# Kernel optimization log

Measured on AMD Instinct MI355X. Metric: run time of the kernel, lower is better.

Reference implementation:

```python
import jax, jax.numpy as jnp
import numpy as np

B, NI, NA, D = 16, 2048, 2048, 256

def setup_inputs() -> dict:
    key = jax.random.key(0)
    k1, k2, k3 = jax.random.split(key, 3)
    input_seq = jax.random.normal(k1, (B, NI, D), dtype=jnp.float32)
    attendee_seq = jax.random.normal(k2, (B, NA, D), dtype=jnp.float32)
    # glorot-ish scale for bilinear weight
    W = jax.random.normal(k3, (D, D), dtype=jnp.float32) * (1.0 / np.sqrt(D))
    return {"input_seq": input_seq, "attendee_seq": attendee_seq, "W": W}

def reference(input_seq, attendee_seq, W):
    # bilinear scores: (x_i W) . a_j   -> [B, NI, NA]
    xW = jnp.einsum('bid,de->bie', input_seq, W)
    scores = jnp.einsum('bie,bje->bij', xW, attendee_seq)
    A = jax.nn.softmax(scores, axis=2)                 # softmax over attendee axis
    # weighted context: sum_j A[b,i,j] * v[b,j,:] -> [B, NI, D]
    attended = jnp.einsum('bij,bjd->bid', A, attendee_seq)
    return attended
```

## Files before the change

kernel.cpp:

```cpp
#include <hip/hip_runtime.h>
#include <hip/hip_bf16.h>

#define BB 16
#define NI 2048
#define NA 2048
#define DD 256
#define KVB 32
#define NT (NA / KVB)

typedef _Float16 half8 __attribute__((ext_vector_type(8)));
typedef __attribute__((ext_vector_type(4))) float f32x4;
typedef __attribute__((ext_vector_type(4))) unsigned int uint4v;

typedef const unsigned int CGU __attribute__((address_space(1)));
typedef unsigned int LU __attribute__((address_space(3)));

static __device__ __forceinline__ unsigned short f2h(float f) {
  union { _Float16 h; unsigned short u; } x; x.h = (_Float16)f; return x.u;
}
static __device__ __forceinline__ float h2f(unsigned short u) {
  union { _Float16 h; unsigned short u; } x; x.u = u; return (float)x.h;
}
static __device__ __forceinline__ unsigned int pk2(float a, float b) {
  return __builtin_bit_cast(unsigned int, __builtin_amdgcn_cvt_pkrtz(a, b));
}
static __device__ __forceinline__ float ex2(float x) {
  return __builtin_amdgcn_exp2f(x);
}
static __device__ __forceinline__ void gload16(const unsigned short* g, unsigned short* l) {
  __builtin_amdgcn_global_load_lds((CGU*)g, (LU*)l, 16, 0, 0);
}

__global__ void prep_kernel(const float* __restrict__ a,
                            unsigned short* __restrict__ kfrag,
                            unsigned short* __restrict__ vfrag,
                            const float* __restrict__ w,
                            unsigned short* __restrict__ wth,
                            unsigned short* __restrict__ wtl) {
  __shared__ float t[64][65];
  int bx = blockIdx.x;
  int tid = threadIdx.x;
  int rr = tid >> 4, c4 = tid & 15;

  if (bx >= 2048) {
    int r = bx - 2048;
    int dt = r >> 2, et = r & 3;
    int d0 = dt * 64, e0 = et * 64;
    int cc = c4 * 4;
#pragma unroll
    for (int k = 0; k < 4; ++k) {
      int row = rr + k * 16;
      float4 v = *(const float4*)(w + (size_t)(d0 + row) * DD + e0 + cc);
      t[row][cc + 0] = v.x; t[row][cc + 1] = v.y; t[row][cc + 2] = v.z; t[row][cc + 3] = v.w;
    }
    __syncthreads();
#pragma unroll
    for (int k = 0; k < 4; ++k) {
      int e = rr + k * 16;
      int eg = e0 + e;
      ushort4 h, l;
      float v0 = t[cc + 0][e]; h.x = f2h(v0); l.x = f2h(v0 - h2f(h.x));
      float v1 = t[cc + 1][e]; h.y = f2h(v1); l.y = f2h(v1 - h2f(h.y));
      float v2 = t[cc + 2][e]; h.z = f2h(v2); l.z = f2h(v2 - h2f(h.z));
      float v3 = t[cc + 3][e]; h.w = f2h(v3); l.w = f2h(v3 - h2f(h.w));
      int dd = d0 + cc;
      int u = dd >> 3, sub = dd & 7;
      size_t off = (size_t)eg * DD + ((u ^ (eg & 7)) * 8) + sub;
      *(ushort4*)(wth + off) = h;
      *(ushort4*)(wtl + off) = l;
    }
    return;
  }

  int b = bx >> 7;
  int r = bx & 127;
  int jt_t = r >> 2, dt_t = r & 3;
  int j0 = jt_t * 64, d0 = dt_t * 64;
#pragma unroll
  for (int k = 0; k < 4; ++k) {
    int row = rr + k * 16;
    int j = j0 + row;
    int d = d0 + c4 * 4;
    float4 v = *(const float4*)(a + ((size_t)b * NA + j) * DD + d);
    ushort4 hh;
    hh.x = f2h(v.x); hh.y = f2h(v.y); hh.z = f2h(v.z); hh.w = f2h(v.w);
    int kt = j >> 5, jtf = (j >> 4) & 1, l16k = j & 15;
    int c = d >> 5, quad = (d >> 3) & 3, e = d & 7;
    *(ushort4*)(kfrag + ((size_t)b * NT + kt) * 8192 + c * 1024 + jtf * 512 +
                (quad * 16 + l16k) * 8 + e) = hh;
    t[row][c4 * 4 + 0] = v.x; t[row][c4 * 4 + 1] = v.y;
    t[row][c4 * 4 + 2] = v.z; t[row][c4 * 4 + 3] = v.w;
  }
  __syncthreads();
#pragma unroll
  for (int k = 0; k < 4; ++k) {
    int dl = rr + k * 16;
    int d = d0 + dl;
    int j = j0 + c4 * 4;
    ushort4 o;
    o.x = f2h(t[c4 * 4 + 0][dl]); o.y = f2h(t[c4 * 4 + 1][dl]);
    o.z = f2h(t[c4 * 4 + 2][dl]); o.w = f2h(t[c4 * 4 + 3][dl]);
    int kt = j >> 5;
    int quad = c4 & 3;
    int jt = (c4 >> 2) & 1;
    int hh_ = (d >> 7) & 1, dtl = (d >> 4) & 7, l16v = d & 15;
    *(ushort4*)(vfrag + ((size_t)b * NT + kt) * 8192 + hh_ * 4096 + dtl * 512 +
                (quad * 16 + l16v) * 8 + jt * 4) = o;
  }
}

__global__ __launch_bounds__(256, 2) void qgemm_kernel(
    const float* __restrict__ x, const unsigned short* __restrict__ wth,
    const unsigned short* __restrict__ wtl, unsigned short* __restrict__ qf) {
  __shared__ unsigned short wb[2][64 * 256];
  const int tid = threadIdx.x;
  const int lane = tid & 63;
  const int wv = tid >> 6;
  const int quad = lane >> 4;
  const int l16 = lane & 15;
  const int m0 = blockIdx.x * 64;

  half8 xf[8];
  {
    const float* xr = x + (size_t)(m0 + wv * 16 + l16) * DD;
#pragma unroll
    for (int c = 0; c < 8; ++c) {
      float4 a = *(const float4*)(xr + c * 32 + quad * 8);
      float4 b = *(const float4*)(xr + c * 32 + quad * 8 + 4);
      half8 v;
      v[0] = (_Float16)a.x; v[1] = (_Float16)a.y; v[2] = (_Float16)a.z; v[3] = (_Float16)a.w;
      v[4] = (_Float16)b.x; v[5] = (_Float16)b.y; v[6] = (_Float16)b.z; v[7] = (_Float16)b.w;
      xf[c] = v;
    }
  }

#pragma unroll 1
  for (int eg = 0; eg < 4; ++eg) {
    uint4 t0[8], t1[8];
    {
      const unsigned short* sh = wth + (size_t)(eg * 64) * DD;
      const unsigned short* sl = wtl + (size_t)(eg * 64) * DD;
#pragma unroll
      for (int i = 0; i < 8; ++i) {
        t0[i] = *(const uint4*)(sh + (i * 256 + tid) * 8);
        t1[i] = *(const uint4*)(sl + (i * 256 + tid) * 8);
      }
    }
    __syncthreads();
#pragma unroll
    for (int i = 0; i < 8; ++i) {
      *(uint4*)(wb[0] + (i * 256 + tid) * 8) = t0[i];
      *(uint4*)(wb[1] + (i * 256 + tid) * 8) = t1[i];
    }
    __syncthreads();
#pragma unroll
    for (int etl = 0; etl < 4; ++etl) {
      int rloc = etl * 16 + l16;
      f32x4 acc; acc[0] = acc[1] = acc[2] = acc[3] = 0.f;
#pragma unroll
      for (int c = 0; c < 8; ++c) {
        int off = rloc * DD + (((4 * c + quad) ^ (rloc & 7)) * 8);
        half8 wh = *(const half8*)(wb[0] + off);
        half8 wl = *(const half8*)(wb[1] + off);
        acc = __builtin_amdgcn_mfma_f32_16x16x32_f16(xf[c], wh, acc, 0, 0, 0);
        acc = __builtin_amdgcn_mfma_f32_16x16x32_f16(xf[c], wl, acc, 0, 0, 0);
      }
      int e = eg * 64 + etl * 16 + l16;
#pragma unroll
      for (int rg = 0; rg < 4; ++rg) {
        qf[(size_t)(m0 + wv * 16 + 4 * quad + rg) * DD + e] = f2h(acc[rg] * 1.44269504f);
      }
    }
  }
}

__global__ __launch_bounds__(256, 4) void attn_kernel(
    const unsigned short* __restrict__ kfrag, const unsigned short* __restrict__ vfrag,
    const unsigned short* __restrict__ qf, float* __restrict__ out) {
  __shared__ unsigned short kls[2][KVB * DD];

  const int tid = threadIdx.x;
  const int lane = tid & 63;
  const int wv = tid >> 6;
  const int p = wv >> 1;
  const int h = wv & 1;
  const int quad = lane >> 4;
  const int l16 = lane & 15;

  int bx = blockIdx.x;
  int lbx = (bx & 7) * 128 + (bx >> 3);
  const int b = lbx >> 6;
  const int qbase = (lbx & 63) * 32 + p * 16;

  const unsigned short* kfb = kfrag + (size_t)b * NT * 8192;

  half8 qh[8];
  {
    const size_t qrow = ((size_t)b * NI + qbase + l16) * DD;
#pragma unroll
    for (int c = 0; c < 8; ++c)
      qh[c] = *(const half8*)(qf + qrow + c * 32 + quad * 8);
  }

  f32x4 acc[8];
#pragma unroll
  for (int dt = 0; dt < 8; ++dt) { acc[dt][0] = 0.f; acc[dt][1] = 0.f; acc[dt][2] = 0.f; acc[dt][3] = 0.f; }
  float m0r = -INFINITY;
  float l0 = 0.f;

  const unsigned short* vp = vfrag + (size_t)b * NT * 8192 + h * 4096 + lane * 8;
  const unsigned short* sp = kfb + 8192 + (wv * 512 + lane * 8);

#pragma unroll
  for (int i = 0; i < 4; ++i) {
    int off = (i * 4 + wv) * 512;
    gload16(kfb + off + lane * 8, &kls[0][off]);
  }
  __syncthreads();

#pragma unroll 1
  for (int kt = 0; kt < NT; ++kt) {
    half8 vb[8];
#pragma unroll
    for (int dt = 0; dt < 8; ++dt)
      vb[dt] = *(const half8*)(vp + dt * 512);

    if (kt + 1 < NT) {
      unsigned short* d = &kls[(kt + 1) & 1][wv * 512];
      gload16(sp + 0 * 2048, d + 0 * 2048);
      gload16(sp + 1 * 2048, d + 1 * 2048);
      gload16(sp + 2 * 2048, d + 2 * 2048);
      gload16(sp + 3 * 2048, d + 3 * 2048);
    }

    const unsigned short* kb = &kls[kt & 1][0];
    f32x4 st0, st1;
    st0[0] = st0[1] = st0[2] = st0[3] = 0.f;
    st1[0] = st1[1] = st1[2] = st1[3] = 0.f;
    __builtin_amdgcn_s_setprio(1);
#pragma unroll
    for (int c = 0; c < 8; ++c) {
      half8 k0 = *(const half8*)(kb + c * 1024 + lane * 8);
      half8 k1 = *(const half8*)(kb + c * 1024 + 512 + lane * 8);
      st0 = __builtin_amdgcn_mfma_f32_16x16x32_f16(k0, qh[c], st0, 0, 0, 0);
      st1 = __builtin_amdgcn_mfma_f32_16x16x32_f16(k1, qh[c], st1, 0, 0, 0);
    }
    __builtin_amdgcn_s_setprio(0);

    float mt = fmaxf(fmaxf(fmaxf(st0[0], st0[1]), fmaxf(st0[2], st0[3])),
                     fmaxf(fmaxf(st1[0], st1[1]), fmaxf(st1[2], st1[3])));
    if (__any(mt > m0r + 11.5416f)) {
      float mr = fmaxf(mt, __shfl_xor(mt, 16));
      mr = fmaxf(mr, __shfl_xor(mr, 32));
      float mn = fmaxf(m0r, mr);
      float sc = ex2(m0r - mn);
      l0 *= sc;
#pragma unroll
      for (int rg = 0; rg < 4; ++rg) {
        float a0 = __shfl(sc, 4 * quad + rg);
#pragma unroll
        for (int dt = 0; dt < 8; ++dt) acc[dt][rg] *= a0;
      }
      m0r = mn;
    }

    float e00 = ex2(st0[0] - m0r), e01 = ex2(st0[1] - m0r);
    float e02 = ex2(st0[2] - m0r), e03 = ex2(st0[3] - m0r);
    float e10 = ex2(st1[0] - m0r), e11 = ex2(st1[1] - m0r);
    float e12 = ex2(st1[2] - m0r), e13 = ex2(st1[3] - m0r);
    l0 += ((e00 + e01) + (e02 + e03)) + ((e10 + e11) + (e12 + e13));
    half8 pa;
    {
      uint4v pau = { pk2(e00, e01), pk2(e02, e03), pk2(e10, e11), pk2(e12, e13) };
      pa = __builtin_bit_cast(half8, pau);
    }

    __builtin_amdgcn_s_setprio(1);
#pragma unroll
    for (int dt = 0; dt < 8; ++dt)
      acc[dt] = __builtin_amdgcn_mfma_f32_16x16x32_f16(pa, vb[dt], acc[dt], 0, 0, 0);
    __builtin_amdgcn_s_setprio(0);

    vp += 8192;
    sp += 8192;
    __syncthreads();
  }

  l0 += __shfl_xor(l0, 16); l0 += __shfl_xor(l0, 32);
  float inv0 = 1.0f / l0;
  size_t ob = ((size_t)b * NI + qbase) * DD + h * 128;
#pragma unroll
  for (int rg = 0; rg < 4; ++rg) {
    float i0 = __shfl(inv0, 4 * quad + rg);
#pragma unroll
    for (int dt = 0; dt < 8; ++dt) {
      int d = dt * 16 + l16;
      out[ob + (size_t)(4 * quad + rg) * DD + d] = acc[dt][rg] * i0;
    }
  }
}

extern "C" void kernel_launch(void* const* d_in, const int* in_sizes, int n_in,
                              void* d_out, int out_size, void* d_ws, size_t ws_size,
                              hipStream_t stream) {
  const float* x = (const float*)d_in[0];
  const float* att = (const float*)d_in[1];
  const float* W = (const float*)d_in[2];
  float* out = (float*)d_out;

  const size_t NE = (size_t)BB * NA * DD;
  unsigned short* w0    = (unsigned short*)d_ws;
  unsigned short* kfrag = w0;
  unsigned short* vfrag = w0 + NE;
  unsigned short* qfp   = w0 + 2 * NE;
  unsigned short* wth   = w0 + 3 * NE;
  unsigned short* wtl   = w0 + 3 * NE + (size_t)DD * DD;

  prep_kernel<<<2064, 256, 0, stream>>>(att, kfrag, vfrag, W, wth, wtl);
  qgemm_kernel<<<512, 256, 0, stream>>>(x, wth, wtl, qfp);
  attn_kernel<<<1024, 256, 0, stream>>>(kfrag, vfrag, qfp, out);
}
```

Before: 197.6 us.

## Switch attention to 32x32x16 MFMA with 64-query blocks and new fragment layouts

Rewrites the attention inner loop to use 32x32x16 MFMA tiles instead of 16x16x32. Each wave now covers 32 query rows, so a block covers 64 queries and the grid halves to 512 blocks. The prep kernel writes K/V fragments in matching layouts, the softmax row-max needs fewer shuffles, and outputs are written as float4. Each K/V tile loaded into LDS now feeds twice as many queries, which cuts K/V traffic per query. In exchange, register pressure rises (16 Q fragments, 4x16 accumulators), occupancy drops to 2 blocks per CU, and the score reduction is split into two accumulators.

```diff
diff --git a/kernel.cpp b/kernel.cpp
--- a/kernel.cpp
+++ b/kernel.cpp
@@ -9,7 +9,7 @@
 #define NT (NA / KVB)
 
 typedef _Float16 half8 __attribute__((ext_vector_type(8)));
-typedef __attribute__((ext_vector_type(4))) float f32x4;
+typedef __attribute__((ext_vector_type(16))) float f32x16;
 typedef __attribute__((ext_vector_type(4))) unsigned int uint4v;
 
 typedef const unsigned int CGU __attribute__((address_space(1)));
@@ -84,10 +84,10 @@
     float4 v = *(const float4*)(a + ((size_t)b * NA + j) * DD + d);
     ushort4 hh;
     hh.x = f2h(v.x); hh.y = f2h(v.y); hh.z = f2h(v.z); hh.w = f2h(v.w);
-    int kt = j >> 5, jtf = (j >> 4) & 1, l16k = j & 15;
-    int c = d >> 5, quad = (d >> 3) & 3, e = d & 7;
-    *(ushort4*)(kfrag + ((size_t)b * NT + kt) * 8192 + c * 1024 + jtf * 512 +
-                (quad * 16 + l16k) * 8 + e) = hh;
+    int kt = j >> 5;
+    int ks = d >> 4;
+    int lk = (j & 31) + 32 * ((d >> 3) & 1);
+    *(ushort4*)(kfrag + (((size_t)b * NT + kt) * 16 + ks) * 512 + lk * 8 + (c4 & 1) * 4) = hh;
     t[row][c4 * 4 + 0] = v.x; t[row][c4 * 4 + 1] = v.y;
     t[row][c4 * 4 + 2] = v.z; t[row][c4 * 4 + 3] = v.w;
   }
@@ -101,11 +101,12 @@
     o.x = f2h(t[c4 * 4 + 0][dl]); o.y = f2h(t[c4 * 4 + 1][dl]);
     o.z = f2h(t[c4 * 4 + 2][dl]); o.w = f2h(t[c4 * 4 + 3][dl]);
     int kt = j >> 5;
-    int quad = c4 & 3;
-    int jt = (c4 >> 2) & 1;
-    int hh_ = (d >> 7) & 1, dtl = (d >> 4) & 7, l16v = d & 15;
-    *(ushort4*)(vfrag + ((size_t)b * NT + kt) * 8192 + hh_ * 4096 + dtl * 512 +
-                (quad * 16 + l16v) * 8 + jt * 4) = o;
+    int hi = c4 & 1;
+    int m = (c4 >> 2) & 1;
+    int ebase = ((c4 >> 1) & 1) * 4;
+    int hh_ = d >> 7, dtl = (d >> 5) & 3;
+    int lv = (d & 31) + 32 * hi;
+    *(ushort4*)(vfrag + ((((((size_t)b * NT + kt) * 2 + hh_) * 4 + dtl) * 2 + m) * 512) + lv * 8 + ebase) = o;
   }
 }
 
@@ -156,6 +157,8 @@
 #pragma unroll
     for (int etl = 0; etl < 4; ++etl) {
       int rloc = etl * 16 + l16;
+      float4 acc4 = make_float4(0.f, 0.f, 0.f, 0.f);
+      typedef __attribute__((ext_vector_type(4))) float f32x4;
       f32x4 acc; acc[0] = acc[1] = acc[2] = acc[3] = 0.f;
 #pragma unroll
       for (int c = 0; c < 8; ++c) {
@@ -165,6 +168,7 @@
         acc = __builtin_amdgcn_mfma_f32_16x16x32_f16(xf[c], wh, acc, 0, 0, 0);
         acc = __builtin_amdgcn_mfma_f32_16x16x32_f16(xf[c], wl, acc, 0, 0, 0);
       }
+      (void)acc4;
       int e = eg * 64 + etl * 16 + l16;
 #pragma unroll
       for (int rg = 0; rg < 4; ++rg) {
@@ -174,7 +178,7 @@
   }
 }
 
-__global__ __launch_bounds__(256, 4) void attn_kernel(
+__global__ __launch_bounds__(256, 2) void attn_kernel(
     const unsigned short* __restrict__ kfrag, const unsigned short* __restrict__ vfrag,
     const unsigned short* __restrict__ qf, float* __restrict__ out) {
   __shared__ unsigned short kls[2][KVB * DD];
@@ -182,33 +186,35 @@
   const int tid = threadIdx.x;
   const int lane = tid & 63;
   const int wv = tid >> 6;
-  const int p = wv >> 1;
+  const int pr = wv >> 1;
   const int h = wv & 1;
-  const int quad = lane >> 4;
-  const int l16 = lane & 15;
+  const int l31 = lane & 31;
+  const int hi = lane >> 5;
 
   int bx = blockIdx.x;
-  int lbx = (bx & 7) * 128 + (bx >> 3);
-  const int b = lbx >> 6;
-  const int qbase = (lbx & 63) * 32 + p * 16;
+  int lbx = (bx & 7) * 64 + (bx >> 3);
+  const int b = lbx >> 5;
+  const int qbase = (lbx & 31) * 64 + pr * 32;
 
   const unsigned short* kfb = kfrag + (size_t)b * NT * 8192;
 
-  half8 qh[8];
+  half8 qh[16];
   {
-    const size_t qrow = ((size_t)b * NI + qbase + l16) * DD;
-#pragma unroll
-    for (int c = 0; c < 8; ++c)
-      qh[c] = *(const half8*)(qf + qrow + c * 32 + quad * 8);
-  }
-
-  f32x4 acc[8];
-#pragma unroll
-  for (int dt = 0; dt < 8; ++dt) { acc[dt][0] = 0.f; acc[dt][1] = 0.f; acc[dt][2] = 0.f; acc[dt][3] = 0.f; }
+    const unsigned short* qr = qf + ((size_t)b * NI + qbase + l31) * DD + hi * 8;
+#pragma unroll
+    for (int ks = 0; ks < 16; ++ks)
+      qh[ks] = *(const half8*)(qr + ks * 16);
+  }
+
+  f32x16 acc[4];
+#pragma unroll
+  for (int dt = 0; dt < 4; ++dt)
+#pragma unroll
+    for (int i = 0; i < 16; ++i) acc[dt][i] = 0.f;
   float m0r = -INFINITY;
   float l0 = 0.f;
 
-  const unsigned short* vp = vfrag + (size_t)b * NT * 8192 + h * 4096 + lane * 8;
+  const unsigned short* vp = vfrag + (((size_t)b * NT * 2 + h) * 4) * 1024 + lane * 8;
   const unsigned short* sp = kfb + 8192 + (wv * 512 + lane * 8);
 
 #pragma unroll
@@ -222,8 +228,8 @@
   for (int kt = 0; kt < NT; ++kt) {
     half8 vb[8];
 #pragma unroll
-    for (int dt = 0; dt < 8; ++dt)
-      vb[dt] = *(const half8*)(vp + dt * 512);
+    for (int i = 0; i < 8; ++i)
+      vb[i] = *(const half8*)(vp + i * 512);
 
     if (kt + 1 < NT) {
       unsigned short* d = &kls[(kt + 1) & 1][wv * 512];
@@ -234,51 +240,60 @@
     }
 
     const unsigned short* kb = &kls[kt & 1][0];
-    f32x4 st0, st1;
-    st0[0] = st0[1] = st0[2] = st0[3] = 0.f;
-    st1[0] = st1[1] = st1[2] = st1[3] = 0.f;
+    f32x16 sA, sB;
+#pragma unroll
+    for (int i = 0; i < 16; ++i) { sA[i] = 0.f; sB[i] = 0.f; }
     __builtin_amdgcn_s_setprio(1);
 #pragma unroll
-    for (int c = 0; c < 8; ++c) {
-      half8 k0 = *(const half8*)(kb + c * 1024 + lane * 8);
-      half8 k1 = *(const half8*)(kb + c * 1024 + 512 + lane * 8);
-      st0 = __builtin_amdgcn_mfma_f32_16x16x32_f16(k0, qh[c], st0, 0, 0, 0);
-      st1 = __builtin_amdgcn_mfma_f32_16x16x32_f16(k1, qh[c], st1, 0, 0, 0);
+    for (int ks = 0; ks < 8; ++ks) {
+      half8 ka = *(const half8*)(kb + ks * 512 + lane * 8);
+      sA = __builtin_amdgcn_mfma_f32_32x32x16_f16(ka, qh[ks], sA, 0, 0, 0);
+    }
+#pragma unroll
+    for (int ks = 8; ks < 16; ++ks) {
+      half8 ka = *(const half8*)(kb + ks * 512 + lane * 8);
+      sB = __builtin_amdgcn_mfma_f32_32x32x16_f16(ka, qh[ks], sB, 0, 0, 0);
     }
     __builtin_amdgcn_s_setprio(0);
-
-    float mt = fmaxf(fmaxf(fmaxf(st0[0], st0[1]), fmaxf(st0[2], st0[3])),
-                     fmaxf(fmaxf(st1[0], st1[1]), fmaxf(st1[2], st1[3])));
+    float p[16];
+#pragma unroll
+    for (int i = 0; i < 16; ++i) p[i] = sA[i] + sB[i];
+
+    float mt = p[0];
+#pragma unroll
+    for (int i = 1; i < 16; ++i) mt = fmaxf(mt, p[i]);
+    mt = fmaxf(mt, __shfl_xor(mt, 32));
     if (__any(mt > m0r + 11.5416f)) {
-      float mr = fmaxf(mt, __shfl_xor(mt, 16));
-      mr = fmaxf(mr, __shfl_xor(mr, 32));
-      float mn = fmaxf(m0r, mr);
+      float mn = fmaxf(m0r, mt);
       float sc = ex2(m0r - mn);
       l0 *= sc;
 #pragma unroll
-      for (int rg = 0; rg < 4; ++rg) {
-        float a0 = __shfl(sc, 4 * quad + rg);
-#pragma unroll
-        for (int dt = 0; dt < 8; ++dt) acc[dt][rg] *= a0;
-      }
+      for (int dt = 0; dt < 4; ++dt)
+#pragma unroll
+        for (int i = 0; i < 16; ++i) acc[dt][i] *= sc;
       m0r = mn;
     }
 
-    float e00 = ex2(st0[0] - m0r), e01 = ex2(st0[1] - m0r);
-    float e02 = ex2(st0[2] - m0r), e03 = ex2(st0[3] - m0r);
-    float e10 = ex2(st1[0] - m0r), e11 = ex2(st1[1] - m0r);
-    float e12 = ex2(st1[2] - m0r), e13 = ex2(st1[3] - m0r);
-    l0 += ((e00 + e01) + (e02 + e03)) + ((e10 + e11) + (e12 + e13));
-    half8 pa;
+#pragma unroll
+    for (int i = 0; i < 16; ++i) p[i] = ex2(p[i] - m0r);
+    float s0 = ((p[0] + p[1]) + (p[2] + p[3])) + ((p[4] + p[5]) + (p[6] + p[7]));
+    float s1 = ((p[8] + p[9]) + (p[10] + p[11])) + ((p[12] + p[13]) + (p[14] + p[15]));
+    l0 += s0 + s1;
+
+    half8 pa0, pa1;
     {
-      uint4v pau = { pk2(e00, e01), pk2(e02, e03), pk2(e10, e11), pk2(e12, e13) };
-      pa = __builtin_bit_cast(half8, pau);
+      uint4v u0 = { pk2(p[0], p[1]), pk2(p[2], p[3]), pk2(p[4], p[5]), pk2(p[6], p[7]) };
+      uint4v u1 = { pk2(p[8], p[9]), pk2(p[10], p[11]), pk2(p[12], p[13]), pk2(p[14], p[15]) };
+      pa0 = __builtin_bit_cast(half8, u0);
+      pa1 = __builtin_bit_cast(half8, u1);
     }
 
     __builtin_amdgcn_s_setprio(1);
 #pragma unroll
-    for (int dt = 0; dt < 8; ++dt)
-      acc[dt] = __builtin_amdgcn_mfma_f32_16x16x32_f16(pa, vb[dt], acc[dt], 0, 0, 0);
+    for (int dt = 0; dt < 4; ++dt) {
+      acc[dt] = __builtin_amdgcn_mfma_f32_32x32x16_f16(vb[dt * 2 + 0], pa0, acc[dt], 0, 0, 0);
+      acc[dt] = __builtin_amdgcn_mfma_f32_32x32x16_f16(vb[dt * 2 + 1], pa1, acc[dt], 0, 0, 0);
+    }
     __builtin_amdgcn_s_setprio(0);
 
     vp += 8192;
@@ -286,16 +301,19 @@
     __syncthreads();
   }
 
-  l0 += __shfl_xor(l0, 16); l0 += __shfl_xor(l0, 32);
+  l0 += __shfl_xor(l0, 32);
   float inv0 = 1.0f / l0;
-  size_t ob = ((size_t)b * NI + qbase) * DD + h * 128;
-#pragma unroll
-  for (int rg = 0; rg < 4; ++rg) {
-    float i0 = __shfl(inv0, 4 * quad + rg);
-#pragma unroll
-    for (int dt = 0; dt < 8; ++dt) {
-      int d = dt * 16 + l16;
-      out[ob + (size_t)(4 * quad + rg) * DD + d] = acc[dt][rg] * i0;
+  float* ob = out + ((size_t)b * NI + qbase + l31) * DD + h * 128 + hi * 4;
+#pragma unroll
+  for (int dt = 0; dt < 4; ++dt) {
+#pragma unroll
+    for (int rq = 0; rq < 4; ++rq) {
+      float4 v;
+      v.x = acc[dt][rq * 4 + 0] * inv0;
+      v.y = acc[dt][rq * 4 + 1] * inv0;
+      v.z = acc[dt][rq * 4 + 2] * inv0;
+      v.w = acc[dt][rq * 4 + 3] * inv0;
+      *(float4*)(ob + dt * 32 + rq * 8) = v;
     }
   }
 }
@@ -318,5 +336,5 @@
 
   prep_kernel<<<2064, 256, 0, stream>>>(att, kfrag, vfrag, W, wth, wtl);
   qgemm_kernel<<<512, 256, 0, stream>>>(x, wth, wtl, qfp);
-  attn_kernel<<<1024, 256, 0, stream>>>(kfrag, vfrag, qfp, out);
-}
+  attn_kernel<<<512, 256, 0, stream>>>(kfrag, vfrag, qfp, out);
+}
```

Result: faster. 182.7 us (-7.6%).
